# Kernel tuning notes

Measured on AMD Instinct MI355X. Metric: run time of the kernel, lower is better.

Reference implementation:

```python
import jax, jax.numpy as jnp
import numpy as np

N = 100000
IN_DIM = 256
HID = 256
EMB = 64
E = 3200000
EPS = 1e-3  # keras BatchNormalization default epsilon


def setup_inputs() -> dict:
    key = jax.random.key(0)
    ks = jax.random.split(key, 8)
    x = jax.random.normal(ks[0], (N, IN_DIM), dtype=jnp.float32)
    edge_row = jax.random.randint(ks[1], (E,), 0, N, dtype=jnp.int32)
    edge_col = jax.random.randint(ks[2], (E,), 0, N, dtype=jnp.int32)
    edge_val = jax.random.uniform(ks[3], (E,), dtype=jnp.float32)
    # glorot-uniform weights
    lim1 = float(np.sqrt(6.0 / (IN_DIM + HID)))
    w1 = jax.random.uniform(ks[4], (IN_DIM, HID), minval=-lim1, maxval=lim1, dtype=jnp.float32)
    lim2 = float(np.sqrt(6.0 / (HID + EMB)))
    w2 = jax.random.uniform(ks[5], (HID, EMB), minval=-lim2, maxval=lim2, dtype=jnp.float32)
    # BN params (inference mode uses moving stats)
    gamma1 = jnp.ones((HID,), jnp.float32)
    beta1 = jnp.zeros((HID,), jnp.float32)
    mean1 = jax.random.normal(ks[6], (HID,), dtype=jnp.float32) * 0.1
    var1 = jnp.ones((HID,), jnp.float32)
    gamma2 = jnp.ones((EMB,), jnp.float32)
    beta2 = jnp.zeros((EMB,), jnp.float32)
    mean2 = jax.random.normal(ks[7], (EMB,), dtype=jnp.float32) * 0.1
    var2 = jnp.ones((EMB,), jnp.float32)
    return dict(x=x, edge_row=edge_row, edge_col=edge_col, edge_val=edge_val,
                w1=w1, w2=w2, gamma1=gamma1, beta1=beta1, mean1=mean1, var1=var1,
                gamma2=gamma2, beta2=beta2, mean2=mean2, var2=var2)


def _spmm(edge_row, edge_col, edge_val, dense):
    # out[i] = sum_{e: row_e == i} val_e * dense[col_e]
    gathered = edge_val[:, None] * dense[edge_col]  # [E, D]
    return jax.ops.segment_sum(gathered, edge_row, num_segments=N)


def _bn_inf(h, gamma, beta, mean, var):
    return (h - mean) * jax.lax.rsqrt(var + EPS) * gamma + beta


def reference(x, edge_row, edge_col, edge_val, w1, w2,
              gamma1, beta1, mean1, var1, gamma2, beta2, mean2, var2):
    # layer 1: A @ (X W1), BN (inference), ReLU; dropout is identity at inference
    h = _spmm(edge_row, edge_col, edge_val, x @ w1)
    h = jax.nn.relu(_bn_inf(h, gamma1, beta1, mean1, var1))
    # layer 2
    z = _spmm(edge_row, edge_col, edge_val, h @ w2)
    z = _bn_inf(z, gamma2, beta2, mean2, var2)
    return z
```

## Files before the change

kernel.cpp:

```cpp
#include <hip/hip_runtime.h>
#include <hip/hip_bf16.h>

constexpr int NN   = 100000;
constexpr int IND  = 256;
constexpr int HIDD = 256;
constexpr int EMBD = 64;
constexpr int EE   = 3200000;
constexpr int CB    = 8;
constexpr int NB    = ((NN - 1) >> CB) + 1;
constexpr int NBP   = 512;
constexpr int CHUNK = 4096;
constexpr int EPT   = CHUNK / 256;
constexpr int NCHUNK = (EE + CHUNK - 1) / CHUNK;
constexpr int MT    = 2;
#define EPS_BN 1e-3f

typedef short  short8  __attribute__((ext_vector_type(8)));
typedef float  floatx4 __attribute__((ext_vector_type(4)));
typedef float  floatx2 __attribute__((ext_vector_type(2)));

static __device__ __forceinline__ unsigned short f2bf(float f) {
  __hip_bfloat16 b = __float2bfloat16(f);
  union { __hip_bfloat16 b; unsigned short u; } cv;
  cv.b = b;
  return cv.u;
}
static __device__ __forceinline__ float bf2f(unsigned short u) {
  return __uint_as_float(((unsigned)u) << 16);
}
static __device__ __forceinline__ unsigned char f2fp8(float f) {
  return (unsigned char)__builtin_amdgcn_cvt_pk_fp8_f32(f, f, 0, false);
}

__global__ __launch_bounds__(256) void swz_w1_kernel(
    const float* __restrict__ w1, unsigned short* __restrict__ w1s) {
  const int t = blockIdx.x * blockDim.x + threadIdx.x;
  const int lane = t & 63;
  const int f = t >> 6;
  const int kt = f >> 4;
  const int nt = f & 15;
  const int n = nt * 16 + (lane & 15);
#pragma unroll
  for (int j = 0; j < 8; ++j) {
    const int k = kt * 32 + (lane >> 4) * 8 + j;
    w1s[(size_t)(f * 64 + lane) * 8 + j] = f2bf(w1[k * HIDD + n]);
  }
}

__global__ __launch_bounds__(256) void swz_w2_kernel(
    const float* __restrict__ w2, unsigned short* __restrict__ w2s) {
  const int t = blockIdx.x * blockDim.x + threadIdx.x;
  const int lane = t & 63;
  const int f = t >> 6;
  const int kt = f >> 2;
  const int nt = f & 3;
  const int n = nt * 16 + (lane & 15);
#pragma unroll
  for (int j = 0; j < 8; ++j) {
    const int k = kt * 32 + (lane >> 4) * 8 + j;
    w2s[(size_t)(f * 64 + lane) * 8 + j] = f2bf(w2[k * EMBD + n]);
  }
}

__global__ __launch_bounds__(512) void gemm1_mfma(
    const float* __restrict__ x, const unsigned short* __restrict__ w1s,
    unsigned char* __restrict__ h0) {
  const int lane = threadIdx.x & 63;
  const int wave = threadIdx.x >> 6;
  const int quad = lane >> 4;
  const int l15  = lane & 15;
  const short8* w1v = (const short8*)w1s;
  short8 bf[2][8];
#pragma unroll
  for (int nt2 = 0; nt2 < 2; ++nt2)
#pragma unroll
    for (int kt = 0; kt < 8; ++kt)
      bf[nt2][kt] = w1v[(size_t)(kt * 16 + wave * 2 + nt2) * 64 + lane];
#pragma unroll
  for (int i = 0; i < MT; ++i) {
    const int m0 = (blockIdx.x * MT + i) * 16;
    const float* ap = x + (size_t)(m0 + l15) * IND + quad * 8;
    short8 af[8];
#pragma unroll
    for (int kt = 0; kt < 8; ++kt) {
      float4 f0 = *(const float4*)(ap + kt * 32);
      float4 f1 = *(const float4*)(ap + kt * 32 + 4);
      short8 a;
      a[0] = (short)f2bf(f0.x); a[1] = (short)f2bf(f0.y);
      a[2] = (short)f2bf(f0.z); a[3] = (short)f2bf(f0.w);
      a[4] = (short)f2bf(f1.x); a[5] = (short)f2bf(f1.y);
      a[6] = (short)f2bf(f1.z); a[7] = (short)f2bf(f1.w);
      af[kt] = a;
    }
    floatx4 c0 = {0.f, 0.f, 0.f, 0.f};
    floatx4 c1 = {0.f, 0.f, 0.f, 0.f};
#pragma unroll
    for (int kt = 0; kt < 8; ++kt) {
      c0 = __builtin_amdgcn_mfma_f32_16x16x32_bf16(af[kt], bf[0][kt], c0, 0, 0, 0);
      c1 = __builtin_amdgcn_mfma_f32_16x16x32_bf16(af[kt], bf[1][kt], c1, 0, 0, 0);
    }
    unsigned char* o = h0 + (size_t)(m0 + quad * 4) * HIDD + wave * 32 + l15;
#pragma unroll
    for (int r = 0; r < 4; ++r) {
      o[(size_t)r * HIDD]      = f2fp8(c0[r]);
      o[(size_t)r * HIDD + 16] = f2fp8(c1[r]);
    }
  }
}

__global__ __launch_bounds__(256) void gemm2_mfma(
    const unsigned short* __restrict__ hb, const unsigned short* __restrict__ w2s,
    unsigned char* __restrict__ z0) {
  const int lane = threadIdx.x & 63;
  const int wave = threadIdx.x >> 6;
  const int quad = lane >> 4;
  const int l15  = lane & 15;
  const short8* w2v = (const short8*)w2s;
  short8 bf[8];
#pragma unroll
  for (int kt = 0; kt < 8; ++kt)
    bf[kt] = w2v[(size_t)(kt * 4 + wave) * 64 + lane];
#pragma unroll
  for (int i = 0; i < MT; ++i) {
    const int m0 = (blockIdx.x * MT + i) * 16;
    const unsigned short* ap = hb + (size_t)(m0 + l15) * HIDD + quad * 8;
    short8 af[8];
#pragma unroll
    for (int kt = 0; kt < 8; ++kt)
      af[kt] = *(const short8*)(ap + kt * 32);
    floatx4 c = {0.f, 0.f, 0.f, 0.f};
#pragma unroll
    for (int kt = 0; kt < 8; ++kt)
      c = __builtin_amdgcn_mfma_f32_16x16x32_bf16(af[kt], bf[kt], c, 0, 0, 0);
    unsigned char* o = z0 + (size_t)(m0 + quad * 4) * EMBD + wave * 16 + l15;
#pragma unroll
    for (int r = 0; r < 4; ++r) o[(size_t)r * EMBD] = f2fp8(c[r]);
  }
}

__global__ __launch_bounds__(256) void histb_kernel(
    const int* __restrict__ row, int* __restrict__ bcnt) {
  __shared__ int lcnt[NB];
  for (int i = threadIdx.x; i < NB; i += 256) lcnt[i] = 0;
  __syncthreads();
  const int base = blockIdx.x * CHUNK;
  const int lim  = min(EE - base, CHUNK);
  for (int i = threadIdx.x; i < lim; i += 256)
    atomicAdd(&lcnt[row[base + i] >> CB], 1);
  __syncthreads();
  for (int i = threadIdx.x; i < NB; i += 256) {
    const int c = lcnt[i];
    if (c) atomicAdd(&bcnt[i * 16], c);
  }
}

__global__ __launch_bounds__(512) void bscan_kernel(
    const int* __restrict__ bcnt, int* __restrict__ bucket_start,
    int* __restrict__ bcur) {
  __shared__ int lds[512];
  int v = (threadIdx.x < NB) ? bcnt[threadIdx.x * 16] : 0;
  lds[threadIdx.x] = v;
  for (int off = 1; off < 512; off <<= 1) {
    __syncthreads();
    int t = (threadIdx.x >= off) ? lds[threadIdx.x - off] : 0;
    __syncthreads();
    lds[threadIdx.x] += t;
  }
  __syncthreads();
  if (threadIdx.x < NB) {
    const int excl = lds[threadIdx.x] - v;
    bucket_start[threadIdx.x] = excl;
    bcur[threadIdx.x * 16] = excl;
  }
  if (threadIdx.x == 0) bucket_start[NB] = EE;
}

__global__ __launch_bounds__(256) void partA_kernel(
    const int* __restrict__ row, const int* __restrict__ col,
    const float* __restrict__ val, int* __restrict__ bcur,
    unsigned long long* __restrict__ staged) {
  __shared__ unsigned long long sbuf[CHUNK];
  __shared__ int cnt[NBP];
  __shared__ int scn[NBP];
  __shared__ int cur[NB];
  __shared__ int gofs[NB];
  const int base = blockIdx.x * CHUNK;
  const int lim  = min(EE - base, CHUNK);
  for (int i = threadIdx.x; i < NBP; i += 256) cnt[i] = 0;
  __syncthreads();
  unsigned long long rec[EPT];
  int bkt[EPT];
#pragma unroll
  for (int j = 0; j < EPT; ++j) {
    const int idx = threadIdx.x + j * 256;
    bkt[j] = -1;
    if (idx < lim) {
      const int e = base + idx;
      const int r = row[e];
      const int c = col[e];
      const unsigned short v = f2bf(val[e]);
      rec[j] = ((unsigned long long)r << 33) | ((unsigned long long)c << 16) | v;
      bkt[j] = r >> CB;
      atomicAdd(&cnt[bkt[j]], 1);
    }
  }
  __syncthreads();
  for (int i = threadIdx.x; i < NBP; i += 256) scn[i] = cnt[i];
  __syncthreads();
  for (int off = 1; off < NBP; off <<= 1) {
    const int i0 = threadIdx.x, i1 = threadIdx.x + 256;
    const int t0 = (i0 >= off) ? scn[i0 - off] : 0;
    const int t1 = (i1 >= off) ? scn[i1 - off] : 0;
    __syncthreads();
    scn[i0] += t0;
    scn[i1] += t1;
    __syncthreads();
  }
  for (int b = threadIdx.x; b < NB; b += 256) cur[b] = scn[b] - cnt[b];
  __syncthreads();
#pragma unroll
  for (int j = 0; j < EPT; ++j)
    if (bkt[j] >= 0) {
      const int p = atomicAdd(&cur[bkt[j]], 1);
      sbuf[p] = rec[j];
    }
  __syncthreads();
  for (int b = threadIdx.x; b < NB; b += 256) {
    const int c = cnt[b];
    const int g = (c > 0) ? atomicAdd(&bcur[b * 16], c) : 0;
    gofs[b] = g - (scn[b] - c);
  }
  __syncthreads();
  for (int s = threadIdx.x; s < lim; s += 256) {
    const unsigned long long rc = sbuf[s];
    const int b = (int)(rc >> (33 + CB));
    staged[(size_t)(gofs[b] + s)] = rc;
  }
}

__global__ __launch_bounds__(256) void partB_kernel(
    const int* __restrict__ bucket_start,
    const unsigned long long* __restrict__ staged,
    int2* __restrict__ edges, int* __restrict__ row_start) {
  __shared__ int cnt[1 << CB];
  __shared__ int ofs[1 << CB];
  const int b  = blockIdx.x;
  const int r0 = b << CB;
  const int rn = min(NN - r0, 1 << CB);
  const int s  = bucket_start[b];
  const int e  = bucket_start[b + 1];
  cnt[threadIdx.x] = 0;
  __syncthreads();
  const unsigned* hi = (const unsigned*)staged;
  for (int p = s + threadIdx.x; p < e; p += 256) {
    const unsigned hw = hi[2 * p + 1];
    const int r = (int)((hw >> 1) & 0x1FFFF);
    atomicAdd(&cnt[r - r0], 1);
  }
  __syncthreads();
  const int v = cnt[threadIdx.x];
  ofs[threadIdx.x] = v;
  for (int off = 1; off < 256; off <<= 1) {
    __syncthreads();
    const int t = (threadIdx.x >= off) ? ofs[threadIdx.x - off] : 0;
    __syncthreads();
    ofs[threadIdx.x] += t;
  }
  __syncthreads();
  const int excl = ofs[threadIdx.x] - v;
  if ((int)threadIdx.x < rn) row_start[r0 + threadIdx.x] = s + excl;
  if (b == NB - 1 && threadIdx.x == 0) row_start[NN] = e;
  __syncthreads();
  cnt[threadIdx.x] = s + excl;
  __syncthreads();
  for (int p = s + threadIdx.x; p < e; p += 256) {
    const unsigned long long rc = staged[p];
    const int r = (int)(rc >> 33);
    const int c = (int)((rc >> 16) & 0x1FFFF);
    const float vv = bf2f((unsigned short)(rc & 0xFFFF));
    const int q = atomicAdd(&cnt[r - r0], 1);
    int2 pk; pk.x = c << 6; pk.y = __float_as_int(vv);
    edges[q] = pk;
  }
}

__global__ __launch_bounds__(256) void spmm1_kernel(
    const unsigned char* __restrict__ h0, const int* __restrict__ row_start,
    const int2* __restrict__ edges,
    const float* __restrict__ gamma, const float* __restrict__ beta,
    const float* __restrict__ mean, const float* __restrict__ var,
    unsigned short* __restrict__ h) {
  const int row  = (blockIdx.x * blockDim.x + threadIdx.x) >> 6;
  const int lane = threadIdx.x & 63;
  const int lane4 = lane * 4;
  const int s = row_start[row];
  const int e = row_start[row + 1];
  floatx2 acc01 = {0.f, 0.f};
  floatx2 acc23 = {0.f, 0.f};
  int p = s;
  for (; p + 8 <= e; p += 8) {
    int2 er[8];
    unsigned gg[8];
#pragma unroll
    for (int j = 0; j < 8; ++j) er[j] = edges[p + j];
#pragma unroll
    for (int j = 0; j < 8; ++j)
      gg[j] = *(const unsigned*)(h0 + ((size_t)(unsigned)er[j].x * 4) + lane4);
#pragma unroll
    for (int j = 0; j < 8; ++j) {
      const float v = __int_as_float(er[j].y);
      floatx2 lo = __builtin_amdgcn_cvt_pk_f32_fp8(gg[j], false);
      floatx2 hi = __builtin_amdgcn_cvt_pk_f32_fp8(gg[j], true);
      acc01 += lo * v;
      acc23 += hi * v;
    }
  }
  for (; p < e; ++p) {
    int2 e0 = edges[p];
    unsigned g0 = *(const unsigned*)(h0 + ((size_t)(unsigned)e0.x * 4) + lane4);
    const float v0 = __int_as_float(e0.y);
    floatx2 lo = __builtin_amdgcn_cvt_pk_f32_fp8(g0, false);
    floatx2 hi = __builtin_amdgcn_cvt_pk_f32_fp8(g0, true);
    acc01 += lo * v0;
    acc23 += hi * v0;
  }
  const int d = lane4;
  float4 g = *(const float4*)(gamma + d);
  float4 b = *(const float4*)(beta + d);
  float4 m = *(const float4*)(mean + d);
  float4 vv = *(const float4*)(var + d);
  ushort4 o;
  o.x = f2bf(fmaxf(fmaf((acc01.x - m.x) * rsqrtf(vv.x + EPS_BN), g.x, b.x), 0.f));
  o.y = f2bf(fmaxf(fmaf((acc01.y - m.y) * rsqrtf(vv.y + EPS_BN), g.y, b.y), 0.f));
  o.z = f2bf(fmaxf(fmaf((acc23.x - m.z) * rsqrtf(vv.z + EPS_BN), g.z, b.z), 0.f));
  o.w = f2bf(fmaxf(fmaf((acc23.y - m.w) * rsqrtf(vv.w + EPS_BN), g.w, b.w), 0.f));
  *(ushort4*)(h + (size_t)row * HIDD + d) = o;
}

__global__ __launch_bounds__(256) void spmm2_kernel(
    const unsigned char* __restrict__ z0, const int* __restrict__ row_start,
    const int2* __restrict__ edges,
    const float* __restrict__ gamma, const float* __restrict__ beta,
    const float* __restrict__ mean, const float* __restrict__ var,
    float* __restrict__ out) {
  const int row  = (blockIdx.x * blockDim.x + threadIdx.x) >> 6;
  const int lane = threadIdx.x & 63;
  const int s = row_start[row];
  const int e = row_start[row + 1];
  float acc = 0.f;
  int p = s;
  for (; p + 8 <= e; p += 8) {
    int2 er[8];
    unsigned char gb[8];
#pragma unroll
    for (int j = 0; j < 8; ++j) er[j] = edges[p + j];
#pragma unroll
    for (int j = 0; j < 8; ++j)
      gb[j] = z0[(size_t)(unsigned)er[j].x + lane];
#pragma unroll
    for (int j = 0; j < 8; ++j)
      acc = fmaf(__int_as_float(er[j].y),
                 __builtin_amdgcn_cvt_f32_fp8((int)gb[j], 0), acc);
  }
  for (; p < e; ++p) {
    int2 e0 = edges[p];
    unsigned char g0 = z0[(size_t)(unsigned)e0.x + lane];
    acc = fmaf(__int_as_float(e0.y), __builtin_amdgcn_cvt_f32_fp8((int)g0, 0), acc);
  }
  float r = fmaf((acc - mean[lane]) * rsqrtf(var[lane] + EPS_BN), gamma[lane],
                 beta[lane]);
  out[(size_t)row * EMBD + lane] = r;
}

extern "C" void kernel_launch(void* const* d_in, const int* in_sizes, int n_in,
                              void* d_out, int out_size, void* d_ws, size_t ws_size,
                              hipStream_t stream) {
  const float* x        = (const float*)d_in[0];
  const int*   edge_row = (const int*)d_in[1];
  const int*   edge_col = (const int*)d_in[2];
  const float* edge_val = (const float*)d_in[3];
  const float* w1       = (const float*)d_in[4];
  const float* w2       = (const float*)d_in[5];
  const float* gamma1   = (const float*)d_in[6];
  const float* beta1    = (const float*)d_in[7];
  const float* mean1    = (const float*)d_in[8];
  const float* var1     = (const float*)d_in[9];
  const float* gamma2   = (const float*)d_in[10];
  const float* beta2    = (const float*)d_in[11];
  const float* mean2    = (const float*)d_in[12];
  const float* var2     = (const float*)d_in[13];
  float* out = (float*)d_out;

  char* ws = (char*)d_ws;
  size_t off = 0;
  auto alloc = [&](size_t bytes) -> void* {
    void* p = ws + off;
    off = (off + bytes + 255) & ~(size_t)255;
    return p;
  };
  unsigned char*  h0  = (unsigned char*)alloc((size_t)NN * HIDD);
  unsigned short* h   = (unsigned short*)alloc((size_t)NN * HIDD * 2);
  unsigned long long* staged = (unsigned long long*)h;
  unsigned char*  z0  = (unsigned char*)alloc((size_t)NN * EMBD);
  unsigned short* w1s = (unsigned short*)alloc((size_t)IND * HIDD * 2);
  unsigned short* w2s = (unsigned short*)alloc((size_t)HIDD * EMBD * 2);
  int*   row_start    = (int*)alloc((size_t)(NN + 1) * 4);
  int*   bcnt         = (int*)alloc((size_t)NB * 16 * 4);
  int*   bcur         = (int*)alloc((size_t)NB * 16 * 4);
  int*   bucket_start = (int*)alloc((size_t)(NB + 1) * 4);
  int2*  edges        = (int2*)alloc((size_t)EE * 8);

  swz_w1_kernel<<<8192 / 256, 256, 0, stream>>>(w1, w1s);
  swz_w2_kernel<<<2048 / 256, 256, 0, stream>>>(w2, w2s);

  hipMemsetAsync(bcnt, 0, (size_t)NB * 16 * 4, stream);
  histb_kernel<<<NCHUNK, 256, 0, stream>>>(edge_row, bcnt);
  bscan_kernel<<<1, 512, 0, stream>>>(bcnt, bucket_start, bcur);
  partA_kernel<<<NCHUNK, 256, 0, stream>>>(
      edge_row, edge_col, edge_val, bcur, staged);
  partB_kernel<<<NB, 256, 0, stream>>>(bucket_start, staged, edges, row_start);

  gemm1_mfma<<<NN / (16 * MT), 512, 0, stream>>>(x, w1s, h0);
  spmm1_kernel<<<NN / 4, 256, 0, stream>>>(h0, row_start, edges,
                                           gamma1, beta1, mean1, var1, h);
  gemm2_mfma<<<NN / (16 * MT), 256, 0, stream>>>(h, w2s, z0);
  spmm2_kernel<<<NN / 4, 256, 0, stream>>>(z0, row_start, edges,
                                           gamma2, beta2, mean2, var2, out);
}
```

Before: 630.1 us.

## Stage A tiles through double-buffered LDS in both MFMA GEMMs

```diff
diff --git a/kernel.cpp b/kernel.cpp
--- a/kernel.cpp
+++ b/kernel.cpp
@@ -12,7 +12,10 @@
 constexpr int CHUNK = 4096;
 constexpr int EPT   = CHUNK / 256;
 constexpr int NCHUNK = (EE + CHUNK - 1) / CHUNK;
-constexpr int MT    = 2;
+constexpr int GMT    = 8;
+constexpr int GROWS  = GMT * 16;
+constexpr int GGRID  = (NN + GROWS - 1) / GROWS;
+constexpr int APITCH = 264;
 #define EPS_BN 1e-3f
 
 typedef short  short8  __attribute__((ext_vector_type(8)));
@@ -65,8 +68,10 @@
 __global__ __launch_bounds__(512) void gemm1_mfma(
     const float* __restrict__ x, const unsigned short* __restrict__ w1s,
     unsigned char* __restrict__ h0) {
-  const int lane = threadIdx.x & 63;
-  const int wave = threadIdx.x >> 6;
+  __shared__ unsigned short sa[2][16][APITCH];
+  const int tid  = threadIdx.x;
+  const int lane = tid & 63;
+  const int wave = tid >> 6;
   const int quad = lane >> 4;
   const int l15  = lane & 15;
   const short8* w1v = (const short8*)w1s;
@@ -76,34 +81,63 @@
 #pragma unroll
     for (int kt = 0; kt < 8; ++kt)
       bf[nt2][kt] = w1v[(size_t)(kt * 16 + wave * 2 + nt2) * 64 + lane];
-#pragma unroll
-  for (int i = 0; i < MT; ++i) {
-    const int m0 = (blockIdx.x * MT + i) * 16;
-    const float* ap = x + (size_t)(m0 + l15) * IND + quad * 8;
-    short8 af[8];
-#pragma unroll
-    for (int kt = 0; kt < 8; ++kt) {
-      float4 f0 = *(const float4*)(ap + kt * 32);
-      float4 f1 = *(const float4*)(ap + kt * 32 + 4);
-      short8 a;
-      a[0] = (short)f2bf(f0.x); a[1] = (short)f2bf(f0.y);
-      a[2] = (short)f2bf(f0.z); a[3] = (short)f2bf(f0.w);
-      a[4] = (short)f2bf(f1.x); a[5] = (short)f2bf(f1.y);
-      a[6] = (short)f2bf(f1.z); a[7] = (short)f2bf(f1.w);
-      af[kt] = a;
-    }
+
+  const int mbase = blockIdx.x * GROWS;
+  const int srow = tid >> 5;
+  const int scol = (tid & 31) * 8;
+
+  auto srcp = [&](int mt) -> const float* {
+    int r = mbase + mt * 16 + srow;
+    if (r >= NN) r = NN - 1;
+    return x + (size_t)r * IND + scol;
+  };
+
+  {
+    const float* p = srcp(0);
+    float4 g0 = *(const float4*)(p);
+    float4 g1 = *(const float4*)(p + 4);
+    short8 s;
+    s[0] = (short)f2bf(g0.x); s[1] = (short)f2bf(g0.y);
+    s[2] = (short)f2bf(g0.z); s[3] = (short)f2bf(g0.w);
+    s[4] = (short)f2bf(g1.x); s[5] = (short)f2bf(g1.y);
+    s[6] = (short)f2bf(g1.z); s[7] = (short)f2bf(g1.w);
+    *(short8*)&sa[0][srow][(tid & 31) * 8] = s;
+  }
+
+#pragma unroll
+  for (int mt = 0; mt < GMT; ++mt) {
+    const int cur = mt & 1;
+    float4 g0, g1;
+    if (mt + 1 < GMT) {
+      const float* p = srcp(mt + 1);
+      g0 = *(const float4*)(p);
+      g1 = *(const float4*)(p + 4);
+    }
+    __syncthreads();
     floatx4 c0 = {0.f, 0.f, 0.f, 0.f};
     floatx4 c1 = {0.f, 0.f, 0.f, 0.f};
 #pragma unroll
     for (int kt = 0; kt < 8; ++kt) {
-      c0 = __builtin_amdgcn_mfma_f32_16x16x32_bf16(af[kt], bf[0][kt], c0, 0, 0, 0);
-      c1 = __builtin_amdgcn_mfma_f32_16x16x32_bf16(af[kt], bf[1][kt], c1, 0, 0, 0);
-    }
-    unsigned char* o = h0 + (size_t)(m0 + quad * 4) * HIDD + wave * 32 + l15;
-#pragma unroll
-    for (int r = 0; r < 4; ++r) {
-      o[(size_t)r * HIDD]      = f2fp8(c0[r]);
-      o[(size_t)r * HIDD + 16] = f2fp8(c1[r]);
+      short8 a = *(const short8*)&sa[cur][l15][quad * 8 + kt * 32];
+      c0 = __builtin_amdgcn_mfma_f32_16x16x32_bf16(a, bf[0][kt], c0, 0, 0, 0);
+      c1 = __builtin_amdgcn_mfma_f32_16x16x32_bf16(a, bf[1][kt], c1, 0, 0, 0);
+    }
+    const int m0 = mbase + mt * 16;
+    if (m0 < NN) {
+      unsigned char* o = h0 + (size_t)(m0 + quad * 4) * HIDD + wave * 32 + l15;
+#pragma unroll
+      for (int r = 0; r < 4; ++r) {
+        o[(size_t)r * HIDD]      = f2fp8(c0[r]);
+        o[(size_t)r * HIDD + 16] = f2fp8(c1[r]);
+      }
+    }
+    if (mt + 1 < GMT) {
+      short8 s;
+      s[0] = (short)f2bf(g0.x); s[1] = (short)f2bf(g0.y);
+      s[2] = (short)f2bf(g0.z); s[3] = (short)f2bf(g0.w);
+      s[4] = (short)f2bf(g1.x); s[5] = (short)f2bf(g1.y);
+      s[6] = (short)f2bf(g1.z); s[7] = (short)f2bf(g1.w);
+      *(short8*)&sa[cur ^ 1][srow][(tid & 31) * 8] = s;
     }
   }
 }
@@ -111,8 +145,10 @@
 __global__ __launch_bounds__(256) void gemm2_mfma(
     const unsigned short* __restrict__ hb, const unsigned short* __restrict__ w2s,
     unsigned char* __restrict__ z0) {
-  const int lane = threadIdx.x & 63;
-  const int wave = threadIdx.x >> 6;
+  __shared__ unsigned short sa[2][16][APITCH];
+  const int tid  = threadIdx.x;
+  const int lane = tid & 63;
+  const int wave = tid >> 6;
   const int quad = lane >> 4;
   const int l15  = lane & 15;
   const short8* w2v = (const short8*)w2s;
@@ -120,21 +156,51 @@
 #pragma unroll
   for (int kt = 0; kt < 8; ++kt)
     bf[kt] = w2v[(size_t)(kt * 4 + wave) * 64 + lane];
-#pragma unroll
-  for (int i = 0; i < MT; ++i) {
-    const int m0 = (blockIdx.x * MT + i) * 16;
-    const unsigned short* ap = hb + (size_t)(m0 + l15) * HIDD + quad * 8;
-    short8 af[8];
-#pragma unroll
-    for (int kt = 0; kt < 8; ++kt)
-      af[kt] = *(const short8*)(ap + kt * 32);
+
+  const int mbase = blockIdx.x * GROWS;
+  const int srow = tid >> 4;
+  const int scol = (tid & 15) * 16;
+
+  auto srcp = [&](int mt) -> const unsigned short* {
+    int r = mbase + mt * 16 + srow;
+    if (r >= NN) r = NN - 1;
+    return hb + (size_t)r * HIDD + scol;
+  };
+
+  {
+    const unsigned short* p = srcp(0);
+    short8 g0 = *(const short8*)(p);
+    short8 g1 = *(const short8*)(p + 8);
+    *(short8*)&sa[0][srow][scol]     = g0;
+    *(short8*)&sa[0][srow][scol + 8] = g1;
+  }
+
+#pragma unroll
+  for (int mt = 0; mt < GMT; ++mt) {
+    const int cur = mt & 1;
+    short8 g0, g1;
+    if (mt + 1 < GMT) {
+      const unsigned short* p = srcp(mt + 1);
+      g0 = *(const short8*)(p);
+      g1 = *(const short8*)(p + 8);
+    }
+    __syncthreads();
     floatx4 c = {0.f, 0.f, 0.f, 0.f};
 #pragma unroll
-    for (int kt = 0; kt < 8; ++kt)
-      c = __builtin_amdgcn_mfma_f32_16x16x32_bf16(af[kt], bf[kt], c, 0, 0, 0);
-    unsigned char* o = z0 + (size_t)(m0 + quad * 4) * EMBD + wave * 16 + l15;
-#pragma unroll
-    for (int r = 0; r < 4; ++r) o[(size_t)r * EMBD] = f2fp8(c[r]);
+    for (int kt = 0; kt < 8; ++kt) {
+      short8 a = *(const short8*)&sa[cur][l15][quad * 8 + kt * 32];
+      c = __builtin_amdgcn_mfma_f32_16x16x32_bf16(a, bf[kt], c, 0, 0, 0);
+    }
+    const int m0 = mbase + mt * 16;
+    if (m0 < NN) {
+      unsigned char* o = z0 + (size_t)(m0 + quad * 4) * EMBD + wave * 16 + l15;
+#pragma unroll
+      for (int r = 0; r < 4; ++r) o[(size_t)r * EMBD] = f2fp8(c[r]);
+    }
+    if (mt + 1 < GMT) {
+      *(short8*)&sa[cur ^ 1][srow][scol]     = g0;
+      *(short8*)&sa[cur ^ 1][srow][scol + 8] = g1;
+    }
   }
 }
 
@@ -420,10 +486,10 @@
       edge_row, edge_col, edge_val, bcur, staged);
   partB_kernel<<<NB, 256, 0, stream>>>(bucket_start, staged, edges, row_start);
 
-  gemm1_mfma<<<NN / (16 * MT), 512, 0, stream>>>(x, w1s, h0);
+  gemm1_mfma<<<GGRID, 512, 0, stream>>>(x, w1s, h0);
   spmm1_kernel<<<NN / 4, 256, 0, stream>>>(h0, row_start, edges,
                                            gamma1, beta1, mean1, var1, h);
-  gemm2_mfma<<<NN / (16 * MT), 256, 0, stream>>>(h, w2s, z0);
+  gemm2_mfma<<<GGRID, 256, 0, stream>>>(h, w2s, z0);
   spmm2_kernel<<<NN / 4, 256, 0, stream>>>(z0, row_start, edges,
                                            gamma2, beta2, mean2, var2, out);
 }
```

New measurement: 545.6 us. -13.4%, faster.
